# Kernel optimization log

Hardware: AMD Instinct MI355X
Metric: run time of the kernel (lower is better)

Reference implementation:

```python
import jax, jax.numpy as jnp
import numpy as np

B = 4096
V_ECC, V_ERR = 16, 12
T = 25
C_T = 32            # temporal_out
F_IN = C_T * T      # 800 = ChebConv in_channels
GCN_OUT = 64
HID2 = 256          # hidden_size * 2


def _ring_edge_index(n):
    # undirected ring (both directions), no self loops -- AHA-segment-style adjacency
    s = np.arange(n); t = (s + 1) % n
    return np.stack([np.concatenate([s, t]), np.concatenate([t, s])]).astype(np.int64)


def setup_inputs() -> dict:
    key = jax.random.key(0)
    ks = iter(jax.random.split(key, 24))
    p = lambda shape, sc=0.05: jax.random.normal(next(ks), shape, jnp.float32) * sc
    return {
        "ecc": jax.random.normal(next(ks), (B, V_ECC, T), jnp.float32),
        "err": jax.random.normal(next(ks), (B, V_ERR, T), jnp.float32),
        "conv_ecc_w": p((C_T, 1, 3)), "conv_ecc_b": p((C_T,)),
        "conv_err_w": p((C_T, 1, 3)), "conv_err_b": p((C_T,)),
        "cheb_ecc_W": p((2, F_IN, GCN_OUT)), "cheb_ecc_b": p((GCN_OUT,)),
        "cheb_err_W": p((2, F_IN, GCN_OUT)), "cheb_err_b": p((GCN_OUT,)),
        "ecc_proj_W": p((V_ECC * GCN_OUT, HID2)), "ecc_proj_b": p((HID2,)),
        "err_proj_W": p((V_ERR * GCN_OUT, HID2)), "err_proj_b": p((HID2,)),
        "attn_W": p((HID2, 1)), "attn_b": p((1,)),
        "fc2_W": p((HID2, 1)), "fc2_b": p((1,)),
        "edge_index_ecc": jnp.asarray(_ring_edge_index(V_ECC)),
        "edge_index_err": jnp.asarray(_ring_edge_index(V_ERR)),
    }


def _temporal_conv(x, w, b):
    # torch Conv1d(1, C_T, kernel=3, padding=1) applied per node, then
    # reshape(B, V, C_T*T) exactly like the torch code (channel-major per node).
    Bv, V, T_ = x.shape
    y = jax.lax.conv_general_dilated(x.reshape(Bv * V, 1, T_), w, (1,), [(1, 1)],
                                     dimension_numbers=("NCH", "OIH", "NCH"))
    y = y + b[None, :, None]
    return y.reshape(Bv, V, -1)  # [B, V, C_T*T]


def _cheb_conv(x, edge_index, W, b):
    # PyG ChebConv(K=2, normalization='sym', lambda_max=2.0):
    #   Lhat = 2 L / lambda_max - I = -D^{-1/2} A D^{-1/2}
    #   out  = Tx0 @ W[0] + Tx1 @ W[1] + b,  Tx0 = x, Tx1 = Lhat x
    # Batched over B with a single segment_sum (replaces the per-sample loop).
    src, dst = edge_index[0], edge_index[1]
    V = x.shape[1]
    deg = jax.ops.segment_sum(jnp.ones(src.shape, jnp.float32), src, num_segments=V)
    dis = jnp.where(deg > 0, jax.lax.rsqrt(jnp.maximum(deg, 1.0)), 0.0)
    w_e = -dis[src] * dis[dst]                        # [E]
    msg = x[:, src, :] * w_e[None, :, None]           # [B, E, F] gather
    Tx1 = jax.ops.segment_sum(msg.transpose(1, 0, 2), dst, num_segments=V)  # [V, B, F]
    Tx1 = Tx1.transpose(1, 0, 2)                      # [B, V, F] scatter-add
    return jnp.einsum("bvf,fo->bvo", x, W[0]) + jnp.einsum("bvf,fo->bvo", Tx1, W[1]) + b


def reference(ecc, err, conv_ecc_w, conv_ecc_b, conv_err_w, conv_err_b,
              cheb_ecc_W, cheb_ecc_b, cheb_err_W, cheb_err_b,
              ecc_proj_W, ecc_proj_b, err_proj_W, err_proj_b,
              attn_W, attn_b, fc2_W, fc2_b, edge_index_ecc, edge_index_err):
    Bv = ecc.shape[0]
    ecc_f = _temporal_conv(ecc, conv_ecc_w, conv_ecc_b)   # [B, 16, 800]
    err_f = _temporal_conv(err, conv_err_w, conv_err_b)   # [B, 12, 800]
    ecc_out = _cheb_conv(ecc_f, edge_index_ecc, cheb_ecc_W, cheb_ecc_b)  # [B, 16, 64]
    err_out = _cheb_conv(err_f, edge_index_err, cheb_err_W, cheb_err_b)  # [B, 12, 64]
    # gated fusion
    ecc_g = ecc_out.reshape(Bv, -1) @ ecc_proj_W + ecc_proj_b  # [B, 256]
    err_g = err_out.reshape(Bv, -1) @ err_proj_W + err_proj_b  # [B, 256]
    attn = jax.nn.sigmoid(jnp.tanh(ecc_g + err_g) @ attn_W + attn_b)  # [B, 1]
    fused = attn * ecc_g + (1.0 - attn) * err_g   # latent_layer (gated path skips fc1)
    x = jax.nn.relu(fused) @ fc2_W + fc2_b        # dropout = identity (eval mode)
    return jax.nn.sigmoid(x)                      # [B, 1]
```

## Files before the change

### kernel.cpp

```cpp
#include <hip/hip_runtime.h>
#include <hip/hip_bf16.h>
#include <math.h>


#define TM 16
#define HID2 256
#define KE 400
#define KR 300
#define CE 13
#define CR 10

#define OFF_A0   6400
#define OFF_B0   6656
#define OFF_CV   6912
#define KBF_ECC  7040
#define KBF_ERR  60288

typedef __attribute__((ext_vector_type(8))) short  short8;
typedef __attribute__((ext_vector_type(4))) float  f32x4;

static __device__ __forceinline__ float ldv(const void* p, int i, bool f32) {
    return f32 ? ((const float*)p)[i]
               : __bfloat162float(((const __hip_bfloat16*)p)[i]);
}

static __device__ __forceinline__ bool detect_f32(const void* ecc) {
    unsigned w = ((const unsigned*)ecc)[threadIdx.x & 63];
    int e0 = (w >> 7) & 0xff, e1 = (w >> 23) & 0xff;
    return __any((e0 >= 141) || (e1 >= 141)) != 0;
}

static __device__ __forceinline__ int bswz(int k, int o) {
    int c = k >> 5, q = (k >> 3) & 3, j = k & 7;
    int nt = o >> 4, li = o & 15;
    return (c * 16 + nt) * 512 + (q * 16 + li) * 8 + j;
}

static __device__ __forceinline__ unsigned pack_bf16(float x0, float x1) {
    __hip_bfloat16 h0 = __float2bfloat16(x0), h1 = __float2bfloat16(x1);
    unsigned u0 = *(unsigned short*)&h0, u1 = *(unsigned short*)&h1;
    return (u1 << 16) | u0;
}

__global__ void precompute1(const void* __restrict__ ecc,
                            const void* __restrict__ conv_ecc_w,
                            const void* __restrict__ conv_err_w,
                            const void* __restrict__ conv_ecc_b,
                            const void* __restrict__ conv_err_b,
                            const void* __restrict__ cheb_ecc_W,
                            const void* __restrict__ cheb_err_W,
                            float* __restrict__ ws) {
    bool f32 = detect_f32(ecc);
    int tid = threadIdx.x, o = tid & 63, cq = tid >> 6;
    __shared__ float s[256];
    if (blockIdx.x < 100) {
        int m = blockIdx.x / 25, tp = blockIdx.x % 25;
        const void* cw = (m < 2) ? conv_ecc_w : conv_err_w;
        const void* W  = (m < 2) ? cheb_ecc_W : cheb_err_W;
        int wofs = (m & 1) * (800 * 64);
        float acc = 0.f;
        for (int cc = 0; cc < 8; ++cc) {
            int c = cq * 8 + cc;
            #pragma unroll
            for (int k = 0; k < 3; ++k) {
                int t = tp + 1 - k;
                if (t >= 0 && t < 25)
                    acc += ldv(cw, c * 3 + k, f32) * ldv(W, wofs + (c * 25 + t) * 64 + o, f32);
            }
        }
        s[tid] = acc;
        __syncthreads();
        if (tid < 64)
            ws[m * 1600 + tp * 64 + o] = s[tid] + s[tid + 64] + s[tid + 128] + s[tid + 192];
    } else {
        int b = blockIdx.x - 100;
        int sig = b / 25, t = b % 25;
        const void* convb = sig ? conv_err_b : conv_ecc_b;
        const void* W     = sig ? cheb_err_W : cheb_ecc_W;
        float p = 0.f;
        for (int cc = 0; cc < 8; ++cc) {
            int c = cq * 8 + cc;
            float bc = ldv(convb, c, f32);
            p += bc * (ldv(W, (c * 25 + t) * 64 + o, f32)
                     - ldv(W, 800 * 64 + (c * 25 + t) * 64 + o, f32));
        }
        s[tid] = p;
        __syncthreads();
        if (tid < 64)
            atomicAdd(&ws[OFF_CV + sig * 64 + o],
                      s[tid] + s[tid + 64] + s[tid + 128] + s[tid + 192]);
    }
}

__global__ void precompute2(const void* __restrict__ ecc,
                            const void* __restrict__ ecc_proj_W,
                            const void* __restrict__ err_proj_W,
                            const void* __restrict__ ecc_proj_b,
                            const void* __restrict__ err_proj_b,
                            const void* __restrict__ cheb_ecc_b,
                            const void* __restrict__ cheb_err_b,
                            float* __restrict__ ws) {
    bool f32 = detect_f32(ecc);
    int tid = threadIdx.x;
    unsigned short* KbE = (unsigned short*)(ws + KBF_ECC);
    unsigned short* KbR = (unsigned short*)(ws + KBF_ERR);
    if (blockIdx.x < 700) {
        int row = blockIdx.x;
        int sig = (row >= KE);
        int lr  = sig ? row - KE : row;
        int v = lr / 25, tp = lr % 25;
        int V = sig ? 12 : 16;
        const void* P = sig ? err_proj_W : ecc_proj_W;
        const float* W0e = ws + (sig ? 3200 : 0)    + tp * 64;
        const float* W1e = ws + (sig ? 4800 : 1600) + tp * 64;
        __shared__ float w0_s[64], w1_s[64], part[512];
        if (tid < 64) { w0_s[tid] = W0e[tid]; w1_s[tid] = W1e[tid]; }
        __syncthreads();
        int o = tid & 255, jh = tid >> 8;
        int vp = (v + 1) % V, vm = (v + V - 1) % V;
        float acc = 0.f, s1 = 0.f;
        #pragma unroll 4
        for (int jj = 0; jj < 32; ++jj) {
            int j = jh * 32 + jj;
            acc += w0_s[j] * ldv(P, (v  * 64 + j) * HID2 + o, f32);
            s1  += w1_s[j] * (ldv(P, (vp * 64 + j) * HID2 + o, f32)
                            + ldv(P, (vm * 64 + j) * HID2 + o, f32));
        }
        part[tid] = acc - 0.5f * s1;
        __syncthreads();
        if (jh == 0) {
            float kval = part[o] + part[o + 256];
            __hip_bfloat16 h = __float2bfloat16(kval);
            (sig ? KbR : KbE)[bswz(lr, o)] = *(unsigned short*)&h;
        }
    } else if (blockIdx.x < 728) {
        int b = blockIdx.x - 700;
        int sig = (b >= 16);
        int v   = sig ? b - 16 : b;
        const void* P     = sig ? err_proj_W : ecc_proj_W;
        const void* chebb = sig ? cheb_err_b : cheb_ecc_b;
        const void* pb    = sig ? err_proj_b : ecc_proj_b;
        __shared__ float cv_s[64], part[512];
        if (tid < 64) cv_s[tid] = ldv(chebb, tid, f32) + ws[OFF_CV + sig * 64 + tid];
        __syncthreads();
        int o = tid & 255, jh = tid >> 8;
        float acc = 0.f;
        #pragma unroll 4
        for (int jj = 0; jj < 32; ++jj) {
            int j = jh * 32 + jj;
            acc += cv_s[j] * ldv(P, (v * 64 + j) * HID2 + o, f32);
        }
        part[tid] = acc;
        __syncthreads();
        if (jh == 0)
            atomicAdd(&ws[(sig ? OFF_B0 : OFF_A0) + o],
                      part[o] + part[o + 256] + ((v == 0) ? ldv(pb, o, f32) : 0.f));
    } else {
        for (int idx = tid; idx < (16 + 20) * 256; idx += 512) {
            if (idx < 16 * 256) KbE[bswz(400 + (idx >> 8), idx & 255)] = 0;
            else {
                int i2 = idx - 16 * 256;
                KbR[bswz(300 + (i2 >> 8), i2 & 255)] = 0;
            }
        }
    }
}

#define XR_DW 3328

__global__ __launch_bounds__(512, 2) void main_gemm(
        const void* __restrict__ ecc, const void* __restrict__ err,
        const void* __restrict__ attn_W, const void* __restrict__ attn_b,
        const void* __restrict__ fc2_W, const void* __restrict__ fc2_b,
        const float* __restrict__ ws, void* __restrict__ out) {
    __shared__ float smem[2 * 16 * 257];
    unsigned* xs = (unsigned*)smem;

    bool f32 = detect_f32(ecc);
    int tid  = threadIdx.x;
    int row0 = blockIdx.x * TM;

    for (int idx = tid; idx < 16 * 208; idx += 512) {
        int r = idx / 208, i2 = idx - r * 208;
        unsigned u = 0;
        if (i2 < 200) {
            if (f32) u = pack_bf16(((const float*)ecc)[(row0 + r) * 400 + 2 * i2],
                                   ((const float*)ecc)[(row0 + r) * 400 + 2 * i2 + 1]);
            else     u = ((const unsigned*)ecc)[(row0 + r) * 200 + i2];
        }
        xs[(i2 >> 4) * 256 + r * 16 + (i2 & 15)] = u;
    }
    for (int idx = tid; idx < 16 * 160; idx += 512) {
        int r = idx / 160, i2 = idx - r * 160;
        unsigned u = 0;
        if (i2 < 150) {
            if (f32) u = pack_bf16(((const float*)err)[(row0 + r) * 300 + 2 * i2],
                                   ((const float*)err)[(row0 + r) * 300 + 2 * i2 + 1]);
            else     u = ((const unsigned*)err)[(row0 + r) * 150 + i2];
        }
        xs[XR_DW + (i2 >> 4) * 256 + r * 16 + (i2 & 15)] = u;
    }
    __syncthreads();

    int wv = tid >> 6, lane = tid & 63;
    int m = lane & 15, quad = lane >> 4;
    int nt0 = wv * 2;

    const short8* KbE = (const short8*)(ws + KBF_ECC);
    const short8* KbR = (const short8*)(ws + KBF_ERR);
    const char* abase = (const char*)smem + m * 64 + quad * 16;

    f32x4 acc_e[2] = {{0.f, 0.f, 0.f, 0.f}, {0.f, 0.f, 0.f, 0.f}};
    f32x4 acc_r[2] = {{0.f, 0.f, 0.f, 0.f}, {0.f, 0.f, 0.f, 0.f}};

    #pragma unroll
    for (int c = 0; c < CE; ++c) {
        short8 a = *(const short8*)(abase + c * 1024);
        #pragma unroll
        for (int t = 0; t < 2; ++t)
            acc_e[t] = __builtin_amdgcn_mfma_f32_16x16x32_bf16(
                a, KbE[(c * 16 + nt0 + t) * 64 + lane], acc_e[t], 0, 0, 0);
    }
    #pragma unroll
    for (int c = 0; c < CR; ++c) {
        short8 a = *(const short8*)(abase + XR_DW * 4 + c * 1024);
        #pragma unroll
        for (int t = 0; t < 2; ++t)
            acc_r[t] = __builtin_amdgcn_mfma_f32_16x16x32_bf16(
                a, KbR[(c * 16 + nt0 + t) * 64 + lane], acc_r[t], 0, 0, 0);
    }
    __syncthreads();

    float* ge_s = smem;
    float* gr_s = smem + 16 * 257;
    #pragma unroll
    for (int t = 0; t < 2; ++t) {
        int col = (nt0 + t) * 16 + m;
        float a0v = ws[OFF_A0 + col], b0v = ws[OFF_B0 + col];
        #pragma unroll
        for (int i = 0; i < 4; ++i) {
            int row = quad * 4 + i;
            ge_s[row * 257 + col] = acc_e[t][i] + a0v;
            gr_s[row * 257 + col] = acc_r[t][i] + b0v;
        }
    }
    __syncthreads();

    float aw[4], fw[4];
    #pragma unroll
    for (int j = 0; j < 4; ++j) {
        aw[j] = ldv(attn_W, lane + 64 * j, f32);
        fw[j] = ldv(fc2_W,  lane + 64 * j, f32);
    }
    float ab = ldv(attn_b, 0, f32), fb = ldv(fc2_b, 0, f32);
    #pragma unroll
    for (int rr = 0; rr < 2; ++rr) {
        int r = wv * 2 + rr;
        float ge[4], gr[4];
        #pragma unroll
        for (int j = 0; j < 4; ++j) {
            ge[j] = ge_s[r * 257 + lane + 64 * j];
            gr[j] = gr_s[r * 257 + lane + 64 * j];
        }
        float p = 0.f;
        #pragma unroll
        for (int j = 0; j < 4; ++j) p += tanhf(ge[j] + gr[j]) * aw[j];
        #pragma unroll
        for (int off = 32; off; off >>= 1) p += __shfl_down(p, off);
        float a = 1.f / (1.f + expf(-(__shfl(p, 0) + ab)));
        float p2 = 0.f;
        #pragma unroll
        for (int j = 0; j < 4; ++j) {
            float fu = a * ge[j] + (1.f - a) * gr[j];
            p2 += fmaxf(fu, 0.f) * fw[j];
        }
        #pragma unroll
        for (int off = 32; off; off >>= 1) p2 += __shfl_down(p2, off);
        if (lane == 0) {
            float vout = 1.f / (1.f + expf(-(p2 + fb)));
            if (f32) ((float*)out)[row0 + r] = vout;
            else     ((__hip_bfloat16*)out)[row0 + r] = __float2bfloat16(vout);
        }
    }
}

extern "C" void kernel_launch(void* const* d_in, const int* in_sizes, int n_in,
                              void* d_out, int out_size, void* d_ws, size_t ws_size,
                              hipStream_t stream) {
    const void* ecc        = d_in[0];
    const void* err        = d_in[1];
    const void* conv_ecc_w = d_in[2];
    const void* conv_ecc_b = d_in[3];
    const void* conv_err_w = d_in[4];
    const void* conv_err_b = d_in[5];
    const void* cheb_ecc_W = d_in[6];
    const void* cheb_ecc_b = d_in[7];
    const void* cheb_err_W = d_in[8];
    const void* cheb_err_b = d_in[9];
    const void* ecc_proj_W = d_in[10];
    const void* ecc_proj_b = d_in[11];
    const void* err_proj_W = d_in[12];
    const void* err_proj_b = d_in[13];
    const void* attn_W     = d_in[14];
    const void* attn_b     = d_in[15];
    const void* fc2_W      = d_in[16];
    const void* fc2_b      = d_in[17];
    float* ws = (float*)d_ws;

    hipMemsetAsync((char*)d_ws + OFF_A0 * 4, 0, (256 + 256 + 128) * 4, stream);
    precompute1<<<150, 256, 0, stream>>>(ecc, conv_ecc_w, conv_err_w, conv_ecc_b,
                                         conv_err_b, cheb_ecc_W, cheb_err_W, ws);
    precompute2<<<729, 512, 0, stream>>>(ecc, ecc_proj_W, err_proj_W, ecc_proj_b,
                                         err_proj_b, cheb_ecc_b, cheb_err_b, ws);
    main_gemm<<<4096 / TM, 512, 0, stream>>>(ecc, err, attn_W, attn_b, fc2_W, fc2_b,
                                             ws, d_out);
}
```

Baseline: 128.1 us.

## Fuse precompute kernels, drop memset and atomics, vectorize bf16 input staging

Merges the two weight-folding precompute kernels into one launch: each of the 700 row blocks now recomputes its own conv-folded Cheb weight slice locally instead of reading it from a prior kernel, and the bias blocks are reduced to two that loop over all nodes and write directly, so the memset and atomics go away. The main GEMM's bf16 input staging uses uint4/uint2 vector loads and stores instead of per-dword copies. This removes two launches and serial dependencies, at the cost of redundant conv-weight folding in every row block and two long serial bias blocks.

Result: slower. 157.4 us (+22.8%).

```diff
diff --git a/kernel.cpp b/kernel.cpp
--- a/kernel.cpp
+++ b/kernel.cpp
@@ -12,7 +12,6 @@
 
 #define OFF_A0   6400
 #define OFF_B0   6656
-#define OFF_CV   6912
 #define KBF_ECC  7040
 #define KBF_ERR  60288
 
@@ -42,119 +41,114 @@
     return (u1 << 16) | u0;
 }
 
-__global__ void precompute1(const void* __restrict__ ecc,
-                            const void* __restrict__ conv_ecc_w,
-                            const void* __restrict__ conv_err_w,
-                            const void* __restrict__ conv_ecc_b,
-                            const void* __restrict__ conv_err_b,
-                            const void* __restrict__ cheb_ecc_W,
-                            const void* __restrict__ cheb_err_W,
-                            float* __restrict__ ws) {
-    bool f32 = detect_f32(ecc);
-    int tid = threadIdx.x, o = tid & 63, cq = tid >> 6;
-    __shared__ float s[256];
-    if (blockIdx.x < 100) {
-        int m = blockIdx.x / 25, tp = blockIdx.x % 25;
-        const void* cw = (m < 2) ? conv_ecc_w : conv_err_w;
-        const void* W  = (m < 2) ? cheb_ecc_W : cheb_err_W;
-        int wofs = (m & 1) * (800 * 64);
-        float acc = 0.f;
-        for (int cc = 0; cc < 8; ++cc) {
-            int c = cq * 8 + cc;
-            #pragma unroll
-            for (int k = 0; k < 3; ++k) {
-                int t = tp + 1 - k;
-                if (t >= 0 && t < 25)
-                    acc += ldv(cw, c * 3 + k, f32) * ldv(W, wofs + (c * 25 + t) * 64 + o, f32);
-            }
-        }
-        s[tid] = acc;
-        __syncthreads();
-        if (tid < 64)
-            ws[m * 1600 + tp * 64 + o] = s[tid] + s[tid + 64] + s[tid + 128] + s[tid + 192];
-    } else {
-        int b = blockIdx.x - 100;
-        int sig = b / 25, t = b % 25;
-        const void* convb = sig ? conv_err_b : conv_ecc_b;
-        const void* W     = sig ? cheb_err_W : cheb_ecc_W;
-        float p = 0.f;
-        for (int cc = 0; cc < 8; ++cc) {
-            int c = cq * 8 + cc;
-            float bc = ldv(convb, c, f32);
-            p += bc * (ldv(W, (c * 25 + t) * 64 + o, f32)
-                     - ldv(W, 800 * 64 + (c * 25 + t) * 64 + o, f32));
-        }
-        s[tid] = p;
-        __syncthreads();
-        if (tid < 64)
-            atomicAdd(&ws[OFF_CV + sig * 64 + o],
-                      s[tid] + s[tid + 64] + s[tid + 128] + s[tid + 192]);
-    }
-}
-
-__global__ void precompute2(const void* __restrict__ ecc,
-                            const void* __restrict__ ecc_proj_W,
-                            const void* __restrict__ err_proj_W,
-                            const void* __restrict__ ecc_proj_b,
-                            const void* __restrict__ err_proj_b,
-                            const void* __restrict__ cheb_ecc_b,
-                            const void* __restrict__ cheb_err_b,
-                            float* __restrict__ ws) {
+__global__ __launch_bounds__(512) void precompute(
+        const void* __restrict__ ecc,
+        const void* __restrict__ conv_ecc_w, const void* __restrict__ conv_err_w,
+        const void* __restrict__ conv_ecc_b, const void* __restrict__ conv_err_b,
+        const void* __restrict__ cheb_ecc_W, const void* __restrict__ cheb_err_W,
+        const void* __restrict__ cheb_ecc_b, const void* __restrict__ cheb_err_b,
+        const void* __restrict__ ecc_proj_W, const void* __restrict__ err_proj_W,
+        const void* __restrict__ ecc_proj_b, const void* __restrict__ err_proj_b,
+        float* __restrict__ ws) {
     bool f32 = detect_f32(ecc);
     int tid = threadIdx.x;
     unsigned short* KbE = (unsigned short*)(ws + KBF_ECC);
     unsigned short* KbR = (unsigned short*)(ws + KBF_ERR);
+    __shared__ float s0[512], s1[512], w0_s[64], w1_s[64], part[512];
+
     if (blockIdx.x < 700) {
         int row = blockIdx.x;
         int sig = (row >= KE);
         int lr  = sig ? row - KE : row;
         int v = lr / 25, tp = lr % 25;
         int V = sig ? 12 : 16;
-        const void* P = sig ? err_proj_W : ecc_proj_W;
-        const float* W0e = ws + (sig ? 3200 : 0)    + tp * 64;
-        const float* W1e = ws + (sig ? 4800 : 1600) + tp * 64;
-        __shared__ float w0_s[64], w1_s[64], part[512];
-        if (tid < 64) { w0_s[tid] = W0e[tid]; w1_s[tid] = W1e[tid]; }
-        __syncthreads();
+        const void* cw = sig ? conv_err_w : conv_ecc_w;
+        const void* W  = sig ? cheb_err_W : cheb_ecc_W;
+        const void* P  = sig ? err_proj_W : ecc_proj_W;
+
+        {
+            int j = tid & 63, cq = tid >> 6;
+            float a0 = 0.f, a1 = 0.f;
+            #pragma unroll
+            for (int cc = 0; cc < 4; ++cc) {
+                int c = cq * 4 + cc;
+                #pragma unroll
+                for (int k = 0; k < 3; ++k) {
+                    int t = tp + 1 - k;
+                    if (t >= 0 && t < 25) {
+                        float cwv = ldv(cw, c * 3 + k, f32);
+                        a0 += cwv * ldv(W, (c * 25 + t) * 64 + j, f32);
+                        a1 += cwv * ldv(W, 800 * 64 + (c * 25 + t) * 64 + j, f32);
+                    }
+                }
+            }
+            s0[tid] = a0; s1[tid] = a1;
+            __syncthreads();
+            if (tid < 64) {
+                float v0 = 0.f, v1 = 0.f;
+                #pragma unroll
+                for (int g = 0; g < 8; ++g) { v0 += s0[tid + 64 * g]; v1 += s1[tid + 64 * g]; }
+                w0_s[tid] = v0; w1_s[tid] = v1;
+            }
+            __syncthreads();
+        }
         int o = tid & 255, jh = tid >> 8;
         int vp = (v + 1) % V, vm = (v + V - 1) % V;
-        float acc = 0.f, s1 = 0.f;
+        float acc = 0.f, sacc = 0.f;
         #pragma unroll 4
         for (int jj = 0; jj < 32; ++jj) {
             int j = jh * 32 + jj;
-            acc += w0_s[j] * ldv(P, (v  * 64 + j) * HID2 + o, f32);
-            s1  += w1_s[j] * (ldv(P, (vp * 64 + j) * HID2 + o, f32)
-                            + ldv(P, (vm * 64 + j) * HID2 + o, f32));
-        }
-        part[tid] = acc - 0.5f * s1;
+            acc  += w0_s[j] * ldv(P, (v  * 64 + j) * HID2 + o, f32);
+            sacc += w1_s[j] * (ldv(P, (vp * 64 + j) * HID2 + o, f32)
+                             + ldv(P, (vm * 64 + j) * HID2 + o, f32));
+        }
+        part[tid] = acc - 0.5f * sacc;
         __syncthreads();
         if (jh == 0) {
             float kval = part[o] + part[o + 256];
             __hip_bfloat16 h = __float2bfloat16(kval);
             (sig ? KbR : KbE)[bswz(lr, o)] = *(unsigned short*)&h;
         }
-    } else if (blockIdx.x < 728) {
-        int b = blockIdx.x - 700;
-        int sig = (b >= 16);
-        int v   = sig ? b - 16 : b;
+    } else if (blockIdx.x < 702) {
+        int sig = blockIdx.x - 700;
+        int V = sig ? 12 : 16;
+        const void* convb = sig ? conv_err_b : conv_ecc_b;
+        const void* W     = sig ? cheb_err_W : cheb_ecc_W;
+        const void* chebb = sig ? cheb_err_b : cheb_ecc_b;
         const void* P     = sig ? err_proj_W : ecc_proj_W;
-        const void* chebb = sig ? cheb_err_b : cheb_ecc_b;
         const void* pb    = sig ? err_proj_b : ecc_proj_b;
-        __shared__ float cv_s[64], part[512];
-        if (tid < 64) cv_s[tid] = ldv(chebb, tid, f32) + ws[OFF_CV + sig * 64 + tid];
-        __syncthreads();
+
+        {
+            int j = tid & 63, g = tid >> 6;
+            float acc = 0.f;
+            for (int q = 0; q < 100; ++q) {
+                int p = g * 100 + q, c = p / 25, t = p % 25;
+                acc += ldv(convb, c, f32)
+                     * (ldv(W, (c * 25 + t) * 64 + j, f32)
+                      - ldv(W, 800 * 64 + (c * 25 + t) * 64 + j, f32));
+            }
+            s0[tid] = acc;
+            __syncthreads();
+            if (tid < 64) {
+                float v0 = 0.f;
+                #pragma unroll
+                for (int gg = 0; gg < 8; ++gg) v0 += s0[tid + 64 * gg];
+                w0_s[tid] = v0 + ldv(chebb, tid, f32);
+            }
+            __syncthreads();
+        }
         int o = tid & 255, jh = tid >> 8;
         float acc = 0.f;
-        #pragma unroll 4
-        for (int jj = 0; jj < 32; ++jj) {
-            int j = jh * 32 + jj;
-            acc += cv_s[j] * ldv(P, (v * 64 + j) * HID2 + o, f32);
-        }
+        for (int v = 0; v < V; ++v)
+            #pragma unroll 4
+            for (int jj = 0; jj < 32; ++jj) {
+                int j = jh * 32 + jj;
+                acc += w0_s[j] * ldv(P, (v * 64 + j) * HID2 + o, f32);
+            }
         part[tid] = acc;
         __syncthreads();
         if (jh == 0)
-            atomicAdd(&ws[(sig ? OFF_B0 : OFF_A0) + o],
-                      part[o] + part[o + 256] + ((v == 0) ? ldv(pb, o, f32) : 0.f));
+            ws[(sig ? OFF_B0 : OFF_A0) + o] = part[o] + part[o + 256] + ldv(pb, o, f32);
     } else {
         for (int idx = tid; idx < (16 + 20) * 256; idx += 512) {
             if (idx < 16 * 256) KbE[bswz(400 + (idx >> 8), idx & 255)] = 0;
@@ -180,25 +174,44 @@
     int tid  = threadIdx.x;
     int row0 = blockIdx.x * TM;
 
-    for (int idx = tid; idx < 16 * 208; idx += 512) {
-        int r = idx / 208, i2 = idx - r * 208;
-        unsigned u = 0;
-        if (i2 < 200) {
-            if (f32) u = pack_bf16(((const float*)ecc)[(row0 + r) * 400 + 2 * i2],
-                                   ((const float*)ecc)[(row0 + r) * 400 + 2 * i2 + 1]);
-            else     u = ((const unsigned*)ecc)[(row0 + r) * 200 + i2];
-        }
-        xs[(i2 >> 4) * 256 + r * 16 + (i2 & 15)] = u;
-    }
-    for (int idx = tid; idx < 16 * 160; idx += 512) {
-        int r = idx / 160, i2 = idx - r * 160;
-        unsigned u = 0;
-        if (i2 < 150) {
-            if (f32) u = pack_bf16(((const float*)err)[(row0 + r) * 300 + 2 * i2],
-                                   ((const float*)err)[(row0 + r) * 300 + 2 * i2 + 1]);
-            else     u = ((const unsigned*)err)[(row0 + r) * 150 + i2];
-        }
-        xs[XR_DW + (i2 >> 4) * 256 + r * 16 + (i2 & 15)] = u;
+    if (!f32) {
+        const uint4* pe4 = (const uint4*)ecc;
+        for (int idx = tid; idx < 16 * 50; idx += 512) {
+            int r = idx / 50, i4 = idx - r * 50, i2 = 4 * i4;
+            uint4 u = pe4[(row0 + r) * 50 + i4];
+            *(uint4*)(xs + (i2 >> 4) * 256 + r * 16 + (i2 & 15)) = u;
+        }
+        if (tid < 32) {
+            int r = tid >> 1, i2 = 200 + (tid & 1) * 4;
+            *(uint4*)(xs + (i2 >> 4) * 256 + r * 16 + (i2 & 15)) = make_uint4(0, 0, 0, 0);
+        }
+        const uint2* pr2 = (const uint2*)err;
+        for (int idx = tid; idx < 16 * 75; idx += 512) {
+            int r = idx / 75, ip = idx - r * 75, i2 = 2 * ip;
+            uint2 u = pr2[(row0 + r) * 75 + ip];
+            *(uint2*)(xs + XR_DW + (i2 >> 4) * 256 + r * 16 + (i2 & 15)) = u;
+        }
+        if (tid < 80) {
+            int r = tid / 5, i2 = 150 + (tid % 5) * 2;
+            *(uint2*)(xs + XR_DW + (i2 >> 4) * 256 + r * 16 + (i2 & 15)) = make_uint2(0, 0);
+        }
+    } else {
+        for (int idx = tid; idx < 16 * 208; idx += 512) {
+            int r = idx / 208, i2 = idx - r * 208;
+            unsigned u = 0;
+            if (i2 < 200)
+                u = pack_bf16(((const float*)ecc)[(row0 + r) * 400 + 2 * i2],
+                              ((const float*)ecc)[(row0 + r) * 400 + 2 * i2 + 1]);
+            xs[(i2 >> 4) * 256 + r * 16 + (i2 & 15)] = u;
+        }
+        for (int idx = tid; idx < 16 * 160; idx += 512) {
+            int r = idx / 160, i2 = idx - r * 160;
+            unsigned u = 0;
+            if (i2 < 150)
+                u = pack_bf16(((const float*)err)[(row0 + r) * 300 + 2 * i2],
+                              ((const float*)err)[(row0 + r) * 300 + 2 * i2 + 1]);
+            xs[XR_DW + (i2 >> 4) * 256 + r * 16 + (i2 & 15)] = u;
+        }
     }
     __syncthreads();
 
@@ -307,11 +320,10 @@
     const void* fc2_b      = d_in[17];
     float* ws = (float*)d_ws;
 
-    hipMemsetAsync((char*)d_ws + OFF_A0 * 4, 0, (256 + 256 + 128) * 4, stream);
-    precompute1<<<150, 256, 0, stream>>>(ecc, conv_ecc_w, conv_err_w, conv_ecc_b,
-                                         conv_err_b, cheb_ecc_W, cheb_err_W, ws);
-    precompute2<<<729, 512, 0, stream>>>(ecc, ecc_proj_W, err_proj_W, ecc_proj_b,
-                                         err_proj_b, cheb_ecc_b, cheb_err_b, ws);
+    precompute<<<703, 512, 0, stream>>>(ecc, conv_ecc_w, conv_err_w, conv_ecc_b,
+                                        conv_err_b, cheb_ecc_W, cheb_err_W,
+                                        cheb_ecc_b, cheb_err_b, ecc_proj_W,
+                                        err_proj_W, ecc_proj_b, err_proj_b, ws);
     main_gemm<<<4096 / TM, 512, 0, stream>>>(ecc, err, attn_W, attn_b, fc2_W, fc2_b,
                                              ws, d_out);
 }
```
